# Kernel optimization log

Measured on AMD Instinct MI355X. Metric: run time of the kernel, lower is better.

The kernel has to match this reference:

```python
import jax, jax.numpy as jnp
import numpy as np
import math

H = 16
DQ = 64
NEG = -1000000000.0


def setup_inputs() -> dict:
    key = jax.random.key(0)
    ks = jax.random.split(key, 8)
    B, S, D = 2, 2048, 1024
    scale = 1.0 / math.sqrt(D)
    return {
        "embedding": jax.random.normal(ks[0], (B, S, D), dtype=jnp.float32),
        "mask": jax.random.randint(ks[1], (B, 1, S), 0, 2, dtype=jnp.int32),
        "Wq": jax.random.normal(ks[2], (D, D), dtype=jnp.float32) * scale,
        "bq": jnp.zeros((D,), dtype=jnp.float32),
        "Wk": jax.random.normal(ks[3], (D, D), dtype=jnp.float32) * scale,
        "bk": jnp.zeros((D,), dtype=jnp.float32),
        "Wv": jax.random.normal(ks[4], (D, D), dtype=jnp.float32) * scale,
        "bv": jnp.zeros((D,), dtype=jnp.float32),
        "Wo": jax.random.normal(ks[5], (D, D), dtype=jnp.float32) * scale,
        "bo": jnp.zeros((D,), dtype=jnp.float32),
    }


def reference(embedding, mask, Wq, bq, Wk, bk, Wv, bv, Wo, bo):
    B, S, D = embedding.shape
    # projections -> [B, H, S, DQ]
    def proj(W, b):
        return (embedding @ W + b).reshape(B, S, H, DQ).transpose(0, 2, 1, 3)
    q, k, v = proj(Wq, bq), proj(Wk, bk), proj(Wv, bv)
    scores = jnp.einsum("bhqd,bhkd->bhqk", q, k) / math.sqrt(DQ)
    m = mask[:, None]  # [B,1,1,S] broadcasts over heads and query positions
    scores = jnp.where(m == 0, NEG, scores)
    attn = jax.nn.softmax(scores, axis=-1)
    x = jnp.einsum("bhqk,bhkd->bhqd", attn, v)
    x = x.transpose(0, 2, 1, 3).reshape(B, S, H * DQ)
    return x @ Wo + bo
```

## Files before the change

kernel.cpp:

```cpp
#include <hip/hip_runtime.h>
#include <stdint.h>

#define B_ 2
#define S_ 2048
#define D_ 1024
#define H_ 16
#define DQ_ 64
#define M_ 4096
#define CLOG2 16.0f
#define NEGB -1000000000.0f

typedef unsigned short ushort_t;
typedef __attribute__((ext_vector_type(8))) short short8;
typedef __attribute__((ext_vector_type(4))) float floatx4;

#if __has_builtin(__builtin_amdgcn_exp2f)
#define EXP2(x) __builtin_amdgcn_exp2f(x)
#else
#define EXP2(x) exp2f(x)
#endif

__device__ __forceinline__ ushort_t f2bf(float f) {
  union { float f; uint32_t u; } v; v.f = f;
  uint32_t r = v.u + 0x7FFFu + ((v.u >> 16) & 1u);
  return (ushort_t)(r >> 16);
}

__device__ __forceinline__ void async16(const ushort_t* g, ushort_t* l) {
  __builtin_amdgcn_global_load_lds(
      (const __attribute__((address_space(1))) uint32_t*)g,
      (__attribute__((address_space(3))) uint32_t*)l, 16, 0, 0);
}


__global__ void k_cvt_emb(const float* __restrict__ in, ushort_t* __restrict__ out) {
  int i = (blockIdx.x * 256 + threadIdx.x) * 4;
  float4 v = *(const float4*)(in + i);
  uint64_t pk = (uint64_t)f2bf(v.x) | ((uint64_t)f2bf(v.y) << 16) |
                ((uint64_t)f2bf(v.z) << 32) | ((uint64_t)f2bf(v.w) << 48);
  *(uint64_t*)(out + i) = pk;
}

__global__ void k_cvt_w(const float* __restrict__ Wq, const float* __restrict__ Wk,
                        const float* __restrict__ Wv, const float* __restrict__ Wo,
                        ushort_t* __restrict__ Wt) {
  const float* W = (blockIdx.z == 0) ? Wq : (blockIdx.z == 1) ? Wk
                 : (blockIdx.z == 2) ? Wv : Wo;
  ushort_t* out = Wt + (size_t)blockIdx.z * D_ * D_;
  __shared__ float t[32][33];
  int k0 = blockIdx.x * 32, n0 = blockIdx.y * 32;
  int tx = threadIdx.x, ty = threadIdx.y;
  for (int r = 0; r < 32; r += 8)
    t[ty + r][tx] = W[(size_t)(k0 + ty + r) * D_ + n0 + tx];
  __syncthreads();
  for (int r = 0; r < 32; r += 8)
    out[(size_t)(n0 + ty + r) * D_ + k0 + tx] = f2bf(t[tx][ty + r]);
}

template <int IM>
__device__ __forceinline__ void gemm_core2(const ushort_t* __restrict__ A,
                                           const ushort_t* __restrict__ Bt,
                                           ushort_t* As, ushort_t* Bs,
                                           int m0, int n0, floatx4 (&acc)[IM][4]) {
  int t = threadIdx.x, lane = t & 63, w = t >> 6;
  int wm = (w >> 1) * (IM * 16), wn = (w & 1) * 64;
  int l15 = lane & 15, quad = lane >> 4;
  int srow8 = (lane >> 3) & 7;
  int sch = ((lane & 7) ^ srow8) * 8;
  const ushort_t* Ag = A + (size_t)(m0 + w * 8 + srow8) * D_ + sch;
  const ushort_t* Bg = Bt + (size_t)(n0 + w * 8 + srow8) * D_ + sch;
  for (int kt = 0; kt < D_; kt += 64) {
    __syncthreads();
#pragma unroll
    for (int c = 0; c < IM; c++)
      async16(Ag + kt + (size_t)c * 32 * D_, As + (c * 32 + w * 8) * 64);
#pragma unroll
    for (int c = 0; c < 4; c++)
      async16(Bg + kt + (size_t)c * 32 * D_, Bs + (c * 32 + w * 8) * 64);
    __syncthreads();
#pragma unroll
    for (int ks = 0; ks < 2; ks++) {
      int ch = ((ks * 4 + quad) ^ (l15 & 7)) * 8;
      short8 a[IM], b[4];
#pragma unroll
      for (int i = 0; i < IM; i++)
        a[i] = *(const short8*)(As + (wm + i * 16 + l15) * 64 + ch);
#pragma unroll
      for (int j = 0; j < 4; j++)
        b[j] = *(const short8*)(Bs + (wn + j * 16 + l15) * 64 + ch);
#pragma unroll
      for (int i = 0; i < IM; i++)
#pragma unroll
        for (int j = 0; j < 4; j++)
          acc[i][j] = __builtin_amdgcn_mfma_f32_16x16x32_bf16(a[i], b[j], acc[i][j], 0, 0, 0);
    }
  }
}

__global__ __launch_bounds__(256, 3) void k_proj(
    const ushort_t* __restrict__ A, const ushort_t* __restrict__ Wt,
    const float* __restrict__ bq, const float* __restrict__ bk,
    const float* __restrict__ bv,
    ushort_t* __restrict__ Q, ushort_t* __restrict__ K, ushort_t* __restrict__ V) {
  __shared__ __align__(16) ushort_t As[128 * 64];
  __shared__ __align__(16) ushort_t Bs[128 * 64];
  int z = blockIdx.z;
  const ushort_t* Bt = Wt + (size_t)z * D_ * D_;
  const float* bias = (z == 0) ? bq : (z == 1) ? bk : bv;
  int m0 = blockIdx.x * 128, n0 = blockIdx.y * 128;
  floatx4 acc[4][4] = {};
  gemm_core2<4>(A, Bt, As, Bs, m0, n0, acc);
  int lane = threadIdx.x & 63, w = threadIdx.x >> 6;
  int wm = (w >> 1) * 64, wn = (w & 1) * 64;
  int quad = lane >> 4, l15 = lane & 15;
  float scale = (z == 0) ? 0.125f * 1.44269504f : 1.0f;
#pragma unroll
  for (int i = 0; i < 4; i++)
#pragma unroll
    for (int j = 0; j < 4; j++) {
      int ncol = n0 + wn + j * 16 + l15;
      float bb = bias[ncol];
      int h = ncol >> 6, dq = ncol & 63;
      int m = m0 + wm + i * 16 + quad * 4;
      int b = m >> 11, s = m & (S_ - 1);
      if (z == 2) {
        uint64_t pk = (uint64_t)f2bf(acc[i][j][0] + bb) |
                      ((uint64_t)f2bf(acc[i][j][1] + bb) << 16) |
                      ((uint64_t)f2bf(acc[i][j][2] + bb) << 32) |
                      ((uint64_t)f2bf(acc[i][j][3] + bb) << 48);
        *(uint64_t*)(V + ((size_t)(b * H_ + h) * DQ_ + dq) * S_ + s) = pk;
      } else {
        ushort_t* dst = (z == 0) ? Q : K;
#pragma unroll
        for (int r = 0; r < 4; r++)
          dst[((size_t)(b * H_ + h) * S_ + (s + r)) * DQ_ + dq] =
              f2bf((acc[i][j][r] + bb) * scale);
      }
    }
}

__global__ __launch_bounds__(256, 4) void k_attn(
    const ushort_t* __restrict__ Q, const ushort_t* __restrict__ Kg,
    const ushort_t* __restrict__ Vt, const int* __restrict__ mask,
    ushort_t* __restrict__ X) {
  int bh = blockIdx.y, b = bh >> 4, h = bh & 15;
  int q0 = blockIdx.x * 64;
  int t = threadIdx.x, lane = t & 63, w = t >> 6;
  int quad = lane >> 4, l15 = lane & 15;
  const ushort_t* Qh = Q + (size_t)bh * S_ * DQ_;
  const ushort_t* Kh = Kg + (size_t)bh * S_ * DQ_;
  const ushort_t* Vh = Vt + (size_t)bh * DQ_ * S_;
  const int* mb = mask + b * S_;

  __shared__ __align__(16) ushort_t Ks[64 * 64];
  __shared__ __align__(16) ushort_t Vs[64 * 64];
  __shared__ __align__(16) ushort_t Ps[4][16 * 72];

  short8 qf[2];
#pragma unroll
  for (int ks = 0; ks < 2; ks++)
    qf[ks] = *(const short8*)(Qh + (size_t)(q0 + w * 16 + l15) * DQ_ +
                              ks * 32 + quad * 8);

  int srow8 = (lane >> 3) & 7;
  int sch = ((lane & 7) ^ srow8) * 8;
  const ushort_t* Kg1 = Kh + (size_t)(w * 8 + srow8) * DQ_ + sch;
  const ushort_t* Vg1 = Vh + (size_t)(w * 8 + srow8) * S_ + sch;

  floatx4 o[4] = {};
  float lpart[4] = {};

  for (int k0 = 0; k0 < S_; k0 += 64) {
    __syncthreads();
    async16(Kg1 + (size_t)k0 * DQ_, Ks + w * 512);
    async16(Kg1 + (size_t)(k0 + 32) * DQ_, Ks + w * 512 + 2048);
    async16(Vg1 + k0, Vs + w * 512);
    async16(Vg1 + (size_t)32 * S_ + k0, Vs + w * 512 + 2048);
    __syncthreads();

    floatx4 sacc[4] = {};
#pragma unroll
    for (int ks = 0; ks < 2; ks++) {
      int ch = ((ks * 4 + quad) ^ (l15 & 7)) * 8;
      short8 kf[4];
#pragma unroll
      for (int j = 0; j < 4; j++)
        kf[j] = *(const short8*)(Ks + (j * 16 + l15) * 64 + ch);
#pragma unroll
      for (int j = 0; j < 4; j++)
        sacc[j] = __builtin_amdgcn_mfma_f32_16x16x32_bf16(qf[ks], kf[j], sacc[j], 0, 0, 0);
    }

    float bj[4];
#pragma unroll
    for (int j = 0; j < 4; j++)
      bj[j] = mb[k0 + j * 16 + l15] ? -CLOG2 : NEGB;

    ushort_t* Pw = Ps[w];
#pragma unroll
    for (int r = 0; r < 4; r++) {
      float ps = 0.0f;
#pragma unroll
      for (int j = 0; j < 4; j++) {
        float p = EXP2(sacc[j][r] + bj[j]);
        ps += p;
        Pw[(quad * 4 + r) * 72 + j * 16 + l15] = f2bf(p);
      }
      lpart[r] += ps;
    }

#pragma unroll
    for (int ks = 0; ks < 2; ks++) {
      int ch = ((ks * 4 + quad) ^ (l15 & 7)) * 8;
      short8 pf, vf[4];
      pf = *(const short8*)(Pw + l15 * 72 + ks * 32 + quad * 8);
#pragma unroll
      for (int jo = 0; jo < 4; jo++)
        vf[jo] = *(const short8*)(Vs + (jo * 16 + l15) * 64 + ch);
#pragma unroll
      for (int jo = 0; jo < 4; jo++)
        o[jo] = __builtin_amdgcn_mfma_f32_16x16x32_bf16(pf, vf[jo], o[jo], 0, 0, 0);
    }
  }

#pragma unroll
  for (int r = 0; r < 4; r++) {
    float l = lpart[r];
    for (int d = 1; d < 16; d <<= 1) l += __shfl_xor(l, d, 64);
    float inv = 1.0f / l;
    int qrow = q0 + w * 16 + quad * 4 + r;
    size_t base = ((size_t)(b * S_ + qrow)) * D_ + h * DQ_;
#pragma unroll
    for (int jo = 0; jo < 4; jo++)
      X[base + jo * 16 + l15] = f2bf(o[jo][r] * inv);
  }
}

__global__ __launch_bounds__(256, 2) void k_oproj(
    const ushort_t* __restrict__ A, const ushort_t* __restrict__ Wt,
    const float* __restrict__ bias, float* __restrict__ C) {
  __shared__ __align__(16) ushort_t As[64 * 64];
  __shared__ __align__(16) ushort_t Bs[128 * 64];
  int m0 = blockIdx.x * 64, n0 = blockIdx.y * 128;
  floatx4 acc[2][4] = {};
  gemm_core2<2>(A, Wt, As, Bs, m0, n0, acc);
  int lane = threadIdx.x & 63, w = threadIdx.x >> 6;
  int wm = (w >> 1) * 32, wn = (w & 1) * 64;
  int quad = lane >> 4, l15 = lane & 15;
#pragma unroll
  for (int i = 0; i < 2; i++)
#pragma unroll
    for (int j = 0; j < 4; j++) {
      int ncol = n0 + wn + j * 16 + l15;
      float bb = bias[ncol];
      int mr = m0 + wm + i * 16 + quad * 4;
#pragma unroll
      for (int r = 0; r < 4; r++)
        C[(size_t)(mr + r) * D_ + ncol] = acc[i][j][r] + bb;
    }
}

extern "C" void kernel_launch(void* const* d_in, const int* in_sizes, int n_in,
                              void* d_out, int out_size, void* d_ws, size_t ws_size,
                              hipStream_t stream) {
  const float* emb  = (const float*)d_in[0];
  const int*   mask = (const int*)d_in[1];
  const float* Wq = (const float*)d_in[2];
  const float* bq = (const float*)d_in[3];
  const float* Wk = (const float*)d_in[4];
  const float* bk = (const float*)d_in[5];
  const float* Wv = (const float*)d_in[6];
  const float* bv = (const float*)d_in[7];
  const float* Wo = (const float*)d_in[8];
  const float* bo = (const float*)d_in[9];
  float* out = (float*)d_out;

  ushort_t* embb = (ushort_t*)d_ws;
  ushort_t* Wt   = embb + (size_t)M_ * D_;
  ushort_t* Qb   = Wt + (size_t)4 * D_ * D_;
  ushort_t* Kb   = Qb + (size_t)M_ * D_;
  ushort_t* Vb   = Kb + (size_t)M_ * D_;
  ushort_t* Xb   = Vb + (size_t)M_ * D_;

  k_cvt_emb<<<dim3(M_ * D_ / 1024), 256, 0, stream>>>(emb, embb);
  k_cvt_w<<<dim3(32, 32, 4), dim3(32, 8), 0, stream>>>(Wq, Wk, Wv, Wo, Wt);
  k_proj<<<dim3(32, 8, 3), 256, 0, stream>>>(embb, Wt, bq, bk, bv, Qb, Kb, Vb);
  k_attn<<<dim3(32, 32), 256, 0, stream>>>(Qb, Kb, Vb, mask, Xb);
  k_oproj<<<dim3(64, 8), 256, 0, stream>>>(Xb, Wt + (size_t)3 * D_ * D_, bo, out);
}
```

Before: 210.8 us.

## Switch attention kernel to 32x32x16 MFMA tiles with 32 query rows per wave

The attention kernel now gives each wave 32 query rows and uses 32x32x16 bf16 MFMA instructions instead of 16x16x32. Each block covers 128 queries, which halves the grid and the number of K/V tile loads per query. This raises compute per LDS load and cuts instruction count. The probability-to-bf16 conversion switches from round-to-nearest to truncation. The costs are more registers (launch bounds lowered to 2), fewer blocks in flight, and slightly less accurate P values.

```diff
diff --git a/kernel.cpp b/kernel.cpp
--- a/kernel.cpp
+++ b/kernel.cpp
@@ -13,6 +13,7 @@
 typedef unsigned short ushort_t;
 typedef __attribute__((ext_vector_type(8))) short short8;
 typedef __attribute__((ext_vector_type(4))) float floatx4;
+typedef __attribute__((ext_vector_type(16))) float floatx16;
 
 #if __has_builtin(__builtin_amdgcn_exp2f)
 #define EXP2(x) __builtin_amdgcn_exp2f(x)
@@ -24,6 +25,11 @@
   union { float f; uint32_t u; } v; v.f = f;
   uint32_t r = v.u + 0x7FFFu + ((v.u >> 16) & 1u);
   return (ushort_t)(r >> 16);
+}
+
+__device__ __forceinline__ ushort_t f2bf_trunc(float f) {
+  union { float f; uint32_t u; } v; v.f = f;
+  return (ushort_t)(v.u >> 16);
 }
 
 __device__ __forceinline__ void async16(const ushort_t* g, ushort_t* l) {
@@ -139,14 +145,14 @@
     }
 }
 
-__global__ __launch_bounds__(256, 4) void k_attn(
+__global__ __launch_bounds__(256, 2) void k_attn(
     const ushort_t* __restrict__ Q, const ushort_t* __restrict__ Kg,
     const ushort_t* __restrict__ Vt, const int* __restrict__ mask,
     ushort_t* __restrict__ X) {
   int bh = blockIdx.y, b = bh >> 4, h = bh & 15;
-  int q0 = blockIdx.x * 64;
   int t = threadIdx.x, lane = t & 63, w = t >> 6;
-  int quad = lane >> 4, l15 = lane & 15;
+  int l31 = lane & 31, hi = lane >> 5;
+  int q0 = blockIdx.x * 128 + w * 32;
   const ushort_t* Qh = Q + (size_t)bh * S_ * DQ_;
   const ushort_t* Kh = Kg + (size_t)bh * S_ * DQ_;
   const ushort_t* Vh = Vt + (size_t)bh * DQ_ * S_;
@@ -154,21 +160,20 @@
 
   __shared__ __align__(16) ushort_t Ks[64 * 64];
   __shared__ __align__(16) ushort_t Vs[64 * 64];
-  __shared__ __align__(16) ushort_t Ps[4][16 * 72];
-
-  short8 qf[2];
-#pragma unroll
-  for (int ks = 0; ks < 2; ks++)
-    qf[ks] = *(const short8*)(Qh + (size_t)(q0 + w * 16 + l15) * DQ_ +
-                              ks * 32 + quad * 8);
+  __shared__ __align__(16) ushort_t Ps[4][32 * 72];
+
+  short8 qf[4];
+#pragma unroll
+  for (int ks = 0; ks < 4; ks++)
+    qf[ks] = *(const short8*)(Qh + (size_t)(q0 + l31) * DQ_ + ks * 16 + hi * 8);
 
   int srow8 = (lane >> 3) & 7;
   int sch = ((lane & 7) ^ srow8) * 8;
   const ushort_t* Kg1 = Kh + (size_t)(w * 8 + srow8) * DQ_ + sch;
   const ushort_t* Vg1 = Vh + (size_t)(w * 8 + srow8) * S_ + sch;
 
-  floatx4 o[4] = {};
-  float lpart[4] = {};
+  floatx16 o[2] = {};
+  float lp[16] = {};
 
   for (int k0 = 0; k0 < S_; k0 += 64) {
     __syncthreads();
@@ -178,61 +183,50 @@
     async16(Vg1 + (size_t)32 * S_ + k0, Vs + w * 512 + 2048);
     __syncthreads();
 
-    floatx4 sacc[4] = {};
-#pragma unroll
-    for (int ks = 0; ks < 2; ks++) {
-      int ch = ((ks * 4 + quad) ^ (l15 & 7)) * 8;
-      short8 kf[4];
-#pragma unroll
-      for (int j = 0; j < 4; j++)
-        kf[j] = *(const short8*)(Ks + (j * 16 + l15) * 64 + ch);
-#pragma unroll
-      for (int j = 0; j < 4; j++)
-        sacc[j] = __builtin_amdgcn_mfma_f32_16x16x32_bf16(qf[ks], kf[j], sacc[j], 0, 0, 0);
-    }
-
-    float bj[4];
-#pragma unroll
-    for (int j = 0; j < 4; j++)
-      bj[j] = mb[k0 + j * 16 + l15] ? -CLOG2 : NEGB;
+    floatx16 s0 = {}, s1 = {};
+#pragma unroll
+    for (int ks = 0; ks < 4; ks++) {
+      int ch = ((ks * 2 + hi) ^ (l31 & 7)) * 8;
+      short8 kf0 = *(const short8*)(Ks + l31 * 64 + ch);
+      short8 kf1 = *(const short8*)(Ks + (32 + l31) * 64 + ch);
+      s0 = __builtin_amdgcn_mfma_f32_32x32x16_bf16(qf[ks], kf0, s0, 0, 0, 0);
+      s1 = __builtin_amdgcn_mfma_f32_32x32x16_bf16(qf[ks], kf1, s1, 0, 0, 0);
+    }
+
+    float b0 = mb[k0 + l31] ? -CLOG2 : NEGB;
+    float b1 = mb[k0 + 32 + l31] ? -CLOG2 : NEGB;
 
     ushort_t* Pw = Ps[w];
 #pragma unroll
-    for (int r = 0; r < 4; r++) {
-      float ps = 0.0f;
-#pragma unroll
-      for (int j = 0; j < 4; j++) {
-        float p = EXP2(sacc[j][r] + bj[j]);
-        ps += p;
-        Pw[(quad * 4 + r) * 72 + j * 16 + l15] = f2bf(p);
-      }
-      lpart[r] += ps;
-    }
-
-#pragma unroll
-    for (int ks = 0; ks < 2; ks++) {
-      int ch = ((ks * 4 + quad) ^ (l15 & 7)) * 8;
-      short8 pf, vf[4];
-      pf = *(const short8*)(Pw + l15 * 72 + ks * 32 + quad * 8);
-#pragma unroll
-      for (int jo = 0; jo < 4; jo++)
-        vf[jo] = *(const short8*)(Vs + (jo * 16 + l15) * 64 + ch);
-#pragma unroll
-      for (int jo = 0; jo < 4; jo++)
-        o[jo] = __builtin_amdgcn_mfma_f32_16x16x32_bf16(pf, vf[jo], o[jo], 0, 0, 0);
+    for (int r = 0; r < 16; r++) {
+      int qrow = (r & 3) + 8 * (r >> 2) + 4 * hi;
+      float p0 = EXP2(s0[r] + b0);
+      float p1 = EXP2(s1[r] + b1);
+      lp[r] += p0 + p1;
+      Pw[qrow * 72 + l31] = f2bf_trunc(p0);
+      Pw[qrow * 72 + 32 + l31] = f2bf_trunc(p1);
+    }
+
+#pragma unroll
+    for (int ks = 0; ks < 4; ks++) {
+      short8 pf = *(const short8*)(Pw + l31 * 72 + ks * 16 + hi * 8);
+      int ch = ((ks * 2 + hi) ^ (l31 & 7)) * 8;
+      short8 vf0 = *(const short8*)(Vs + l31 * 64 + ch);
+      short8 vf1 = *(const short8*)(Vs + (32 + l31) * 64 + ch);
+      o[0] = __builtin_amdgcn_mfma_f32_32x32x16_bf16(pf, vf0, o[0], 0, 0, 0);
+      o[1] = __builtin_amdgcn_mfma_f32_32x32x16_bf16(pf, vf1, o[1], 0, 0, 0);
     }
   }
 
 #pragma unroll
-  for (int r = 0; r < 4; r++) {
-    float l = lpart[r];
-    for (int d = 1; d < 16; d <<= 1) l += __shfl_xor(l, d, 64);
+  for (int r = 0; r < 16; r++) {
+    float l = lp[r];
+    for (int d = 1; d < 32; d <<= 1) l += __shfl_xor(l, d, 64);
     float inv = 1.0f / l;
-    int qrow = q0 + w * 16 + quad * 4 + r;
+    int qrow = q0 + (r & 3) + 8 * (r >> 2) + 4 * hi;
     size_t base = ((size_t)(b * S_ + qrow)) * D_ + h * DQ_;
-#pragma unroll
-    for (int jo = 0; jo < 4; jo++)
-      X[base + jo * 16 + l15] = f2bf(o[jo][r] * inv);
+    X[base + l31] = f2bf(o[0][r] * inv);
+    X[base + 32 + l31] = f2bf(o[1][r] * inv);
   }
 }
 
@@ -285,6 +279,6 @@
   k_cvt_emb<<<dim3(M_ * D_ / 1024), 256, 0, stream>>>(emb, embb);
   k_cvt_w<<<dim3(32, 32, 4), dim3(32, 8), 0, stream>>>(Wq, Wk, Wv, Wo, Wt);
   k_proj<<<dim3(32, 8, 3), 256, 0, stream>>>(embb, Wt, bq, bk, bv, Qb, Kb, Vb);
-  k_attn<<<dim3(32, 32), 256, 0, stream>>>(Qb, Kb, Vb, mask, Xb);
+  k_attn<<<dim3(16, 32), 256, 0, stream>>>(Qb, Kb, Vb, mask, Xb);
   k_oproj<<<dim3(64, 8), 256, 0, stream>>>(Xb, Wt + (size_t)3 * D_ * D_, bo, out);
 }
```

After: 201.5 us. 1.05x faster.
